# Kernel tuning notes

Measured on AMD Instinct MI355X. Metric: run time of the kernel, lower is better.

Reference implementation:

```python
import jax, jax.numpy as jnp
import numpy as np

# pywt db3 analysis filters (dec_lo, dec_hi)
DB3_LO = np.array([0.035226291882100656, -0.08544127388224149, -0.13501102001039084,
                   0.4598775021193313, 0.8068915093133388, 0.3326705529509569], dtype=np.float32)
DB3_HI = np.array([-0.3326705529509569, 0.8068915093133388, -0.4598775021193313,
                   -0.13501102001039084, 0.08544127388224149, 0.035226291882100656], dtype=np.float32)
L_FILT = 6
J_LEVELS = 3
EPS = 1e-8


def _dwt_level(x):
    """One analysis level, zero-padding ('zero' mode, matches pywt/pytorch_wavelets).
    x: [B, N] -> (low [B, M], high [B, M]) with M = floor((N + L - 1) / 2).
    Uses true convolution (filters flipped) of the full zero-extended signal,
    downsampled at odd full-conv indices, implemented as one strided conv."""
    k = jnp.asarray(np.stack([DB3_LO[::-1], DB3_HI[::-1]])[:, None, :])  # [2,1,L]
    y = jax.lax.conv_general_dilated(x[:, None, :].astype(jnp.float32), k,
                                     window_strides=(2,),
                                     padding=[(L_FILT - 2, L_FILT - 1)])  # [B,2,M]
    return y[:, 0, :], y[:, 1, :]


def _dwt_stats(signals):
    """signals: [B, N]. Returns (mean of final low band, sum over levels of L2 norm
    of each high band) per row -- exactly what the torch loop computes per entity."""
    x = signals
    high_energy = jnp.zeros(signals.shape[0], signals.dtype)
    for _ in range(J_LEVELS):
        lo, hi = _dwt_level(x)
        high_energy = high_energy + jnp.sqrt(jnp.sum(hi * hi, axis=-1))
        x = lo
    return jnp.mean(x, axis=-1), high_energy


def _dirichlet_weight(key, low, high):
    a1 = jnp.clip(low, 1e-6)
    a2 = jnp.clip(high, 1e-6)
    s = a1 + a2
    a1, a2 = a1 / s, a2 / s
    # first component of Dirichlet([10*a1, 10*a2]) ~ Beta(10*a1, 10*a2)
    return jax.random.beta(key, 10.0 * a1, 10.0 * a2)


def setup_inputs() -> dict:
    key = jax.random.key(0)
    k1, k2, k3 = jax.random.split(key, 3)
    U, I, NNZ = 16384, 8192, 1000000
    user_idx = jax.random.randint(k1, (NNZ,), 0, U, dtype=jnp.int32)
    item_idx = jax.random.randint(k2, (NNZ,), 0, I, dtype=jnp.int32)
    values = jax.random.uniform(k3, (NNZ,), dtype=jnp.float32)
    return {"user_idx": user_idx, "item_idx": item_idx, "values": values,
            "num_users": U, "num_items": I}


def reference(user_idx, item_idx, values, num_users, num_items):
    # item popularity
    counts = jax.ops.segment_sum(jnp.ones_like(values), item_idx, num_segments=num_items)
    log_counts = jnp.log1p(counts)
    pop = jax.ops.segment_sum(values * log_counts[item_idx], item_idx, num_segments=num_items)
    pop = pop / (jnp.linalg.norm(pop) + EPS)
    # user activity
    act = jax.ops.segment_sum(values / jnp.log1p(pop[item_idx] + EPS),
                              user_idx, num_segments=num_users)
    act = act / (jnp.linalg.norm(act) + EPS)
    # batched dense signals + DWT (replaces per-entity python loop)
    Su = jnp.zeros((num_users, num_items), values.dtype).at[user_idx, item_idx].set(
        values * (1.0 + act[user_idx]))
    u_low, u_high = _dwt_stats(Su)
    Si = jnp.zeros((num_items, num_users), values.dtype).at[item_idx, user_idx].set(
        values * (1.0 + pop[item_idx]))
    i_low, i_high = _dwt_stats(Si)
    ku, ki = jax.random.split(jax.random.key(42))
    upw = _dirichlet_weight(ku, u_low, u_high)
    ipw = _dirichlet_weight(ki, i_low, i_high)
    return (upw, 1.0 - upw, ipw, 1.0 - ipw, act, pop)
```

## Files before the change

### kernel.cpp

```cpp
#include <hip/hip_runtime.h>
#include <stdint.h>

#define PARTITIONABLE 1

typedef unsigned long long ull;

#define NUM_U 16384
#define NUM_I 8192
#define CAP_U 160
#define CAP_I 256

#define OFF_UPW 0
#define OFF_UMW 16384
#define OFF_IPW 32768
#define OFF_IMW 40960
#define OFF_ACT 49152
#define OFF_POP 65536

struct K2 { uint32_t a, b; };

__host__ __device__ inline void tf2x32(uint32_t k0, uint32_t k1, uint32_t& x0, uint32_t& x1) {
  const uint32_t ks2 = k0 ^ k1 ^ 0x1BD11BDAu;
  x0 += k0; x1 += k1;
#define TF_R(r) { x0 += x1; x1 = (x1 << (r)) | (x1 >> (32 - (r))); x1 ^= x0; }
  TF_R(13) TF_R(15) TF_R(26) TF_R(6)
  x0 += k1; x1 += ks2 + 1u;
  TF_R(17) TF_R(29) TF_R(16) TF_R(24)
  x0 += ks2; x1 += k0 + 2u;
  TF_R(13) TF_R(15) TF_R(26) TF_R(6)
  x0 += k0; x1 += k1 + 3u;
  TF_R(17) TF_R(29) TF_R(16) TF_R(24)
  x0 += k1; x1 += ks2 + 4u;
  TF_R(13) TF_R(15) TF_R(26) TF_R(6)
  x0 += ks2; x1 += k0 + 5u;
#undef TF_R
}

__host__ __device__ inline K2 tf_enc(K2 k, uint32_t x0, uint32_t x1) {
  tf2x32(k.a, k.b, x0, x1);
  K2 r; r.a = x0; r.b = x1; return r;
}

__host__ __device__ inline void split2(K2 k, K2& c0, K2& c1) {
#if PARTITIONABLE
  c0 = tf_enc(k, 0u, 0u);
  c1 = tf_enc(k, 0u, 1u);
#else
  K2 p = tf_enc(k, 0u, 2u);
  K2 q = tf_enc(k, 1u, 3u);
  c0.a = p.a; c0.b = q.a;
  c1.a = p.b; c1.b = q.b;
#endif
}

__device__ inline void split3(K2 k, K2& c0, K2& c1, K2& c2) {
#if PARTITIONABLE
  c0 = tf_enc(k, 0u, 0u);
  c1 = tf_enc(k, 0u, 1u);
  c2 = tf_enc(k, 0u, 2u);
#else
  K2 p = tf_enc(k, 0u, 3u);
  K2 q = tf_enc(k, 1u, 4u);
  K2 r = tf_enc(k, 2u, 5u);
  c0.a = p.a; c0.b = q.a;
  c1.a = r.a; c1.b = p.b;
  c2.a = q.b; c2.b = r.b;
#endif
}

__device__ inline uint32_t draw_bits(K2 k) {
  K2 e = tf_enc(k, 0u, 0u);
#if PARTITIONABLE
  return e.a ^ e.b;
#else
  return e.a;
#endif
}

__device__ inline K2 elem_key(K2 k, uint32_t i, uint32_t B) {
#if PARTITIONABLE
  return tf_enc(k, 0u, i);
#else
  if (i < (B >> 1)) {
    K2 p = tf_enc(k, 2u * i, B + 2u * i);
    K2 q = tf_enc(k, 2u * i + 1u, B + 2u * i + 1u);
    K2 r; r.a = p.a; r.b = q.a; return r;
  } else {
    uint32_t j = 2u * i - B;
    K2 p = tf_enc(k, j, 2u * i);
    K2 q = tf_enc(k, j + 1u, 2u * i + 1u);
    K2 r; r.a = p.b; r.b = q.b; return r;
  }
#endif
}

__device__ inline float u01_bits(uint32_t b) {
  return __uint_as_float((b >> 9) | 0x3F800000u) - 1.0f;
}

__device__ inline float erfinv_f32(float x) {
  float w = -log1pf(-x * x);
  float p;
  if (w < 5.0f) {
    w = w - 2.5f;
    p = 2.81022636e-08f;
    p = fmaf(p, w, 3.43273939e-07f);
    p = fmaf(p, w, -3.5233877e-06f);
    p = fmaf(p, w, -4.39150654e-06f);
    p = fmaf(p, w, 0.00021858087f);
    p = fmaf(p, w, -0.00125372503f);
    p = fmaf(p, w, -0.00417768164f);
    p = fmaf(p, w, 0.246640727f);
    p = fmaf(p, w, 1.50140941f);
  } else {
    w = sqrtf(w) - 3.0f;
    p = -0.000200214257f;
    p = fmaf(p, w, 0.000100950558f);
    p = fmaf(p, w, 0.00134934322f);
    p = fmaf(p, w, -0.00367342844f);
    p = fmaf(p, w, 0.00573950773f);
    p = fmaf(p, w, -0.0076224613f);
    p = fmaf(p, w, 0.00943887047f);
    p = fmaf(p, w, 1.00167406f);
    p = fmaf(p, w, 2.83297682f);
  }
  return p * x;
}

__device__ float log_gamma_sample(K2 key, float alpha_orig) {
  const bool boost = (alpha_orig >= 1.0f);
  const float alpha = boost ? alpha_orig : (alpha_orig + 1.0f);
  const float d = alpha - 0.33333334f;
  const float c = 0.33333334f / sqrtf(d);

  K2 k0, sub;
  split2(key, k0, sub);
  const float u_boost = u01_bits(draw_bits(sub));

  K2 kcur = k0;
  float X = 0.0f, V = 1.0f, U = 2.0f;
  while ((U >= 1.0f - 0.0331f * (X * X)) &&
         (logf(U) >= X * 0.5f + d * ((1.0f - V) + logf(V)))) {
    K2 knext, xk, Uk;
    split3(kcur, knext, xk, Uk);
    kcur = knext;
    float x, v;
    K2 ik = xk;
    do {
      K2 in0, isub;
      split2(ik, in0, isub);
      ik = in0;
      float f = u01_bits(draw_bits(isub));
      float u = fmaxf(-0.99999994f, f * 2.0f + (-0.99999994f));
      x = 1.41421356f * erfinv_f32(u);
      v = 1.0f + x * c;
    } while (v <= 0.0f);
    X = x * x;
    V = (v * v) * v;
    U = u01_bits(draw_bits(Uk));
  }
  float lg = logf(d * V);
  if (!boost) lg += log1pf(-u_boost) / alpha_orig;
  return lg;
}


__global__ __launch_bounds__(256) void init_kernel(ull* __restrict__ nrm2pair,
                                                   ull* __restrict__ fills, int nfill) {
  int i = blockIdx.x * 256 + threadIdx.x;
  if (i < 2) nrm2pair[i] = 0ull;
  if (i < nfill) fills[i] = 0ull;
}

__global__ __launch_bounds__(256) void count_fill_kernel(
    const int* __restrict__ user, const int* __restrict__ item, int n,
    int* __restrict__ fu, int* __restrict__ fi,
    uint32_t* __restrict__ lu, uint32_t* __restrict__ li) {
  for (int k = blockIdx.x * 256 + threadIdx.x; k < n; k += gridDim.x * 256) {
    int it = item[k];
    int q = atomicAdd(&fi[it], 1);
    if (q < CAP_I) li[(size_t)it * CAP_I + q] = (uint32_t)k;
    int u = user[k];
    int p = atomicAdd(&fu[u], 1);
    if (p < CAP_U) lu[(size_t)u * CAP_U + p] = (uint32_t)k;
  }
}

__global__ __launch_bounds__(256) void pop_wave_kernel(
    const int* __restrict__ fi, const uint32_t* __restrict__ li,
    const float* __restrict__ values,
    float* __restrict__ pop, double* __restrict__ nrm2) {
  __shared__ float red[4];
  int lane = threadIdx.x & 63, wid = threadIdx.x >> 6;
  int i = blockIdx.x * 4 + wid;
  int cnt = fi[i];
  int cr = cnt < CAP_I ? cnt : CAP_I;
  long long s = 0;
  for (int e = lane; e < cr; e += 64)
    s += (long long)llrintf(values[li[(size_t)i * CAP_I + e]] * 4294967296.0f);
  for (int o = 32; o > 0; o >>= 1) s += __shfl_down(s, o);
  if (lane == 0) {
    float svf = (float)((double)(ull)s * (1.0 / 4294967296.0));
    float p = svf * log1pf((float)cnt);
    pop[i] = p;
    red[wid] = p * p;
  }
  __syncthreads();
  if (threadIdx.x == 0)
    atomicAdd(nrm2, (double)(red[0] + red[1] + red[2] + red[3]));
}

__global__ __launch_bounds__(256) void act_wave_kernel(
    const int* __restrict__ fu, const uint32_t* __restrict__ lu,
    const int* __restrict__ item, const float* __restrict__ values,
    const float* __restrict__ pop, const double* __restrict__ nrm2_pop,
    float* __restrict__ act, double* __restrict__ nrm2) {
  __shared__ float red[4];
  int lane = threadIdx.x & 63, wid = threadIdx.x >> 6;
  int u = blockIdx.x * 4 + wid;
  int cnt = fu[u];
  int cr = cnt < CAP_U ? cnt : CAP_U;
  const float nrmp = sqrtf((float)(*nrm2_pop));
  const float dnp = nrmp + 1e-8f;
  long long s = 0;
  for (int e = lane; e < cr; e += 64) {
    uint32_t k = lu[(size_t)u * CAP_U + e];
    float pn = pop[item[k]] / dnp;
    float term = values[k] / log1pf(pn + 1e-8f);
    s += (long long)llrintf(term * 16777216.0f);
  }
  for (int o = 32; o > 0; o >>= 1) s += __shfl_down(s, o);
  if (lane == 0) {
    float a = (float)((double)(ull)s * (1.0 / 16777216.0));
    act[u] = a;
    red[wid] = a * a;
  }
  __syncthreads();
  if (threadIdx.x == 0)
    atomicAdd(nrm2, (double)(red[0] + red[1] + red[2] + red[3]));
}

__device__ inline uint32_t evencomp(uint32_t x) {
  x = (x | (x >> 1)) & 0x55555555u;
  x = (x | (x >> 1)) & 0x33333333u;
  x = (x | (x >> 2)) & 0x0F0F0F0Fu;
  x = (x | (x >> 4)) & 0x00FF00FFu;
  x = (x | (x >> 8)) & 0x0000FFFFu;
  return x;
}
template <int NWIN>
__device__ inline uint32_t hword(const uint32_t* B, int i) {
  uint32_t a = (2 * i < NWIN) ? B[2 * i] : 0u;
  uint32_t b = (2 * i + 1 < NWIN) ? B[2 * i + 1] : 0u;
  return evencomp(a) | (evencomp(b) << 16);
}
template <int NWIN>
__device__ inline uint32_t tword(const uint32_t* B, int w) {
  uint32_t h = hword<NWIN>(B, w);
  uint32_t hp = (w > 0) ? hword<NWIN>(B, w - 1) : 0u;
  return h | (h << 1) | (h << 2) | (hp >> 31) | (hp >> 30);
}

template <int NWORDS>
__device__ inline int scan_bits(const uint32_t* __restrict__ W, uint16_t* __restrict__ P,
                                int tid, int* __restrict__ isc, int* __restrict__ tot) {
  constexpr int WPT = (NWORDS + 255) / 256;
  __syncthreads();
  uint32_t w[WPT];
  int v = 0;
#pragma unroll
  for (int j = 0; j < WPT; ++j) {
    int idx = tid * WPT + j;
    w[j] = (idx < NWORDS) ? W[idx] : 0u;
    v += __popc(w[j]);
  }
  int lane = tid & 63, wid = tid >> 6;
  int incl = v;
  for (int off = 1; off < 64; off <<= 1) {
    int y = __shfl_up(incl, off, 64);
    if (lane >= off) incl += y;
  }
  if (lane == 63) isc[wid] = incl;
  __syncthreads();
  int base = 0;
  for (int ww = 0; ww < wid; ++ww) base += isc[ww];
  int run = base + incl - v;
#pragma unroll
  for (int j = 0; j < WPT; ++j) {
    int idx = tid * WPT + j;
    if (idx < NWORDS) P[idx] = (uint16_t)run;
    run += __popc(w[j]);
  }
  if (tid == 255) *tot = run;
  __syncthreads();
  return *tot;
}

template <int NWORDS>
__device__ inline void build_wl(const uint32_t* __restrict__ T, const uint16_t* __restrict__ P,
                                uint16_t* __restrict__ wl, int tid) {
  for (int w = tid; w < NWORDS; w += 256) {
    uint32_t bits = T[w];
    int r0 = P[w], i = 0;
    while (bits) {
      int b = __ffs(bits) - 1; bits &= bits - 1u;
      wl[r0 + i] = (uint16_t)((w << 5) + b);
      ++i;
    }
  }
}

template <int NIN>
__device__ inline void gather6(const uint32_t* __restrict__ B, const uint16_t* __restrict__ P,
                               const float* __restrict__ V, int m,
                               float& lo_o, float& hi_o) {
  int c0 = 2 * m - 4; c0 = c0 < 0 ? 0 : c0;
  int c1 = 2 * m + 1; c1 = c1 > NIN - 1 ? NIN - 1 : c1;
  int w0 = c0 >> 5, w1 = c1 >> 5;
  uint32_t b0 = B[w0];
  uint32_t mlo = ~((1u << (c0 & 31)) - 1u);
  uint32_t mhi = (uint32_t)(((uint64_t)1u << ((c1 & 31) + 1)) - 1u);
  uint32_t sel0, sel1; uint32_t b1 = 0;
  if (w1 == w0) { sel0 = b0 & mlo & mhi; sel1 = 0u; }
  else { b1 = B[w1]; sel0 = b0 & mlo; sel1 = b1 & mhi; }
  float tv0 = 0.0f, tv1 = 0.0f, tv2 = 0.0f, tv3 = 0.0f, tv4 = 0.0f, tv5 = 0.0f;
  int tp1 = 2 * m + 1;
  uint32_t s = sel0;
  while (s) {
    int b = __ffs(s) - 1; s &= s - 1u;
    int c = (w0 << 5) + b;
    int idx = (int)P[w0] + __popc(b0 & ((1u << b) - 1u));
    float v = V[idx];
    int t = tp1 - c;
    if (t == 0) tv0 = v; else if (t == 1) tv1 = v; else if (t == 2) tv2 = v;
    else if (t == 3) tv3 = v; else if (t == 4) tv4 = v; else tv5 = v;
  }
  s = sel1;
  while (s) {
    int b = __ffs(s) - 1; s &= s - 1u;
    int c = (w1 << 5) + b;
    int idx = (int)P[w1] + __popc(b1 & ((1u << b) - 1u));
    float v = V[idx];
    int t = tp1 - c;
    if (t == 0) tv0 = v; else if (t == 1) tv1 = v; else if (t == 2) tv2 = v;
    else if (t == 3) tv3 = v; else if (t == 4) tv4 = v; else tv5 = v;
  }
  float lo = 0.0f, hi = 0.0f;
  lo += 0.035226291882100656f * tv0;  hi += -0.3326705529509569f * tv0;
  lo += -0.08544127388224149f * tv1;  hi += 0.8068915093133388f * tv1;
  lo += -0.13501102001039084f * tv2;  hi += -0.4598775021193313f * tv2;
  lo += 0.4598775021193313f * tv3;    hi += -0.13501102001039084f * tv3;
  lo += 0.8068915093133388f * tv4;    hi += 0.08544127388224149f * tv4;
  lo += 0.3326705529509569f * tv5;    hi += 0.035226291882100656f * tv5;
  lo_o = lo; hi_o = hi;
}

__device__ inline int rank_of(const uint32_t* __restrict__ B, const uint16_t* __restrict__ P,
                              int m) {
  int w = m >> 5;
  return (int)P[w] + __popc(B[w] & ((1u << (m & 31)) - 1u));
}

constexpr int align4c(int x) { return (x + 3) & ~3; }
constexpr int cmax(int a, int b) { return a > b ? a : b; }

constexpr int dwt_shm_bytes(int NCOLS, int M1, int M2, int M3, int CAP) {
  int NW = NCOLS / 32, NW1 = (M1 + 31) / 32, NW2 = (M2 + 31) / 32, NW3 = (M3 + 31) / 32;
  int SZ_RB = cmax(cmax(align4c(NW * 4 + NW * 2), align4c(NW2 * 4 + 4 * CAP * 2)),
                   align4c(5 * CAP * 2));
  int SZ_RC = cmax(align4c(NW1 * 4 + NW1 * 2), align4c(NW3 * 4 + NW3 * 2 + NW2 * 2));
  return (M1 + 12) * 4 + CAP * 4 + SZ_RB + SZ_RC + align4c(3 * CAP * 2) + 64;
}

template <int NCOLS, int M1, int M2, int M3, int CAP>
__global__ __launch_bounds__(256) void dwt_rows_kernel(
    const uint32_t* __restrict__ klist, const int* __restrict__ rowlen,
    const int* __restrict__ colsrc, const float* __restrict__ values,
    const float* __restrict__ scale_raw, const double* __restrict__ nrm2,
    float* __restrict__ low_out, float* __restrict__ high_out,
    float* __restrict__ out, int outoff) {
  static_assert(CAP <= 256, "register-carry staging requires CAP <= blockDim");
  constexpr int NW = NCOLS / 32;
  constexpr int NW1 = (M1 + 31) / 32;
  constexpr int NW2 = (M2 + 31) / 32;
  constexpr int NW3 = (M3 + 31) / 32;
  constexpr uint32_t MK1 = (M1 & 31) ? ((1u << (M1 & 31)) - 1u) : 0xFFFFFFFFu;
  constexpr uint32_t MK2 = (M2 & 31) ? ((1u << (M2 & 31)) - 1u) : 0xFFFFFFFFu;
  constexpr uint32_t MK3 = (M3 & 31) ? ((1u << (M3 & 31)) - 1u) : 0xFFFFFFFFu;
  constexpr int SZ_RB = cmax(cmax(align4c(NW * 4 + NW * 2), align4c(NW2 * 4 + 4 * CAP * 2)),
                             align4c(5 * CAP * 2));
  constexpr int SZ_RC = cmax(align4c(NW1 * 4 + NW1 * 2), align4c(NW3 * 4 + NW3 * 2 + NW2 * 2));

  extern __shared__ char smroot[];
  float* buf = (float*)smroot;
  char* pA = smroot + (M1 + 12) * 4;
  int* slot = (int*)pA;
  float* sval = (float*)pA;
  char* pB = pA + CAP * 4;
  uint32_t* bitmap = (uint32_t*)pB;
  uint16_t* prefix = (uint16_t*)(pB + NW * 4);
  uint32_t* T2 = (uint32_t*)pB;
  uint16_t* wl2 = (uint16_t*)(pB + NW2 * 4);
  uint16_t* wl3 = (uint16_t*)pB;
  char* pC = pB + SZ_RB;
  uint32_t* T1 = (uint32_t*)pC;
  uint16_t* p1 = (uint16_t*)(pC + NW1 * 4);
  uint32_t* T3 = (uint32_t*)pC;
  uint16_t* p3 = (uint16_t*)(pC + NW3 * 4);
  uint16_t* p2 = (uint16_t*)(pC + NW3 * 4 + NW3 * 2);
  char* pD = pC + SZ_RC;
  uint16_t* wl1 = (uint16_t*)pD;
  char* pE = pD + align4c(3 * CAP * 2);
  int* isc = (int*)pE;
  int* tot = isc + 4;
  float* red = (float*)pE;

  const int r = blockIdx.x;
  const int tid = threadIdx.x;
  const float nrm = sqrtf((float)(*nrm2));
  const float snv = scale_raw[r] / (nrm + 1e-8f);
  const float scale = 1.0f + snv;
  if (tid == 0) out[outoff + r] = snv;
  int n = rowlen[r];
  if (n > CAP) n = CAP;

  {
    constexpr int NB4 = (M1 + 12) / 4;
    float4 z; z.x = 0.0f; z.y = 0.0f; z.z = 0.0f; z.w = 0.0f;
    for (int i = tid; i < NB4; i += 256) ((float4*)buf)[i] = z;
    for (int i = NB4 * 4 + tid; i < M1 + 12; i += 256) buf[i] = 0.0f;
  }
  for (int i = tid; i < NW; i += 256) bitmap[i] = 0u;
  if (tid < CAP) slot[tid] = 0;
  __syncthreads();

  const bool have = tid < n;
  uint32_t my_k = 0; int my_c = 0; float my_v = 0.0f;
  if (have) {
    my_k = klist[(size_t)r * CAP + tid];
    my_c = colsrc[my_k];
    my_v = values[my_k] * scale;
    atomicOr(&bitmap[my_c >> 5], 1u << (my_c & 31));
  }
  scan_bits<NW>(bitmap, prefix, tid, isc, tot);

  int my_rank = 0;
  if (have) {
    my_rank = rank_of(bitmap, prefix, my_c);
    atomicMax(&slot[my_rank], (int)my_k + 1);
  }
  __syncthreads();

  if (have && slot[my_rank] == (int)my_k + 1) sval[my_rank] = my_v;
  for (int w = tid; w < NW1; w += 256) {
    uint32_t t = tword<NW>(bitmap, w);
    if (w == NW1 - 1) t &= MK1;
    T1[w] = t;
  }
  const int n1 = scan_bits<NW1>(T1, p1, tid, isc, tot);
  build_wl<NW1>(T1, p1, wl1, tid);
  __syncthreads();

  float h1 = 0.0f;
  for (int idx = tid; idx < n1; idx += 256) {
    int m = wl1[idx];
    float lo, hi;
    gather6<NCOLS>(bitmap, prefix, sval, m, lo, hi);
    buf[4 + m] = lo;
    h1 += hi * hi;
  }
  __syncthreads();

  for (int w = tid; w < NW2; w += 256) {
    uint32_t t = tword<NW1>(T1, w);
    if (w == NW2 - 1) t &= MK2;
    T2[w] = t;
  }
  const int n2 = scan_bits<NW2>(T2, p2, tid, isc, tot);
  build_wl<NW2>(T2, p2, wl2, tid);
  for (int w = tid; w < NW3; w += 256) {
    uint32_t t = tword<NW2>(T2, w);
    if (w == NW3 - 1) t &= MK3;
    T3[w] = t;
  }
  __syncthreads();

  float h2 = 0.0f;
  {
    int nb = (n2 + 255) >> 8;
    for (int b = 0; b < nb; ++b) {
      int idx = (b << 8) + tid;
      bool ok = idx < n2;
      int m = ok ? wl2[idx] : 0;
      const float* s = buf + 2 * m + 5;
      float x0 = s[0], x1 = s[-1], x2 = s[-2], x3 = s[-3], x4 = s[-4], x5 = s[-5];
      __syncthreads();
      if (ok) {
        float lo = 0.0f, hi = 0.0f;
        lo += 0.035226291882100656f * x0;  hi += -0.3326705529509569f * x0;
        lo += -0.08544127388224149f * x1;  hi += 0.8068915093133388f * x1;
        lo += -0.13501102001039084f * x2;  hi += -0.4598775021193313f * x2;
        lo += 0.4598775021193313f * x3;    hi += -0.13501102001039084f * x3;
        lo += 0.8068915093133388f * x4;    hi += 0.08544127388224149f * x4;
        lo += 0.3326705529509569f * x5;    hi += 0.035226291882100656f * x5;
        buf[4 + m] = lo;
        h2 += hi * hi;
      }
    }
  }
  __syncthreads();
  for (int idx = tid; idx < n1; idx += 256) {
    int m = wl1[idx];
    if (m < M2 && !((T2[m >> 5] >> (m & 31)) & 1u)) buf[4 + m] = 0.0f;
  }
  if (tid < 8) buf[4 + M2 + tid] = 0.0f;

  const int n3 = scan_bits<NW3>(T3, p3, tid, isc, tot);
  build_wl<NW3>(T3, p3, wl3, tid);
  __syncthreads();

  float h3 = 0.0f, slo = 0.0f;
  for (int idx = tid; idx < n3; idx += 256) {
    int m = wl3[idx];
    const float* s = buf + 2 * m + 5;
    float x0 = s[0], x1 = s[-1], x2 = s[-2], x3 = s[-3], x4 = s[-4], x5 = s[-5];
    float lo = 0.0f, hi = 0.0f;
    lo += 0.035226291882100656f * x0;  hi += -0.3326705529509569f * x0;
    lo += -0.08544127388224149f * x1;  hi += 0.8068915093133388f * x1;
    lo += -0.13501102001039084f * x2;  hi += -0.4598775021193313f * x2;
    lo += 0.4598775021193313f * x3;    hi += -0.13501102001039084f * x3;
    lo += 0.8068915093133388f * x4;    hi += 0.08544127388224149f * x4;
    lo += 0.3326705529509569f * x5;    hi += 0.035226291882100656f * x5;
    slo += lo;
    h3 += hi * hi;
  }

  for (int o = 32; o > 0; o >>= 1) {
    h1 += __shfl_down(h1, o);
    h2 += __shfl_down(h2, o);
    h3 += __shfl_down(h3, o);
    slo += __shfl_down(slo, o);
  }
  __syncthreads();
  int w = tid >> 6, lane = tid & 63;
  if (lane == 0) { red[w] = h1; red[4 + w] = h2; red[8 + w] = h3; red[12 + w] = slo; }
  __syncthreads();
  if (tid == 0) {
    float s1 = red[0] + red[1] + red[2] + red[3];
    float s2 = red[4] + red[5] + red[6] + red[7];
    float s3 = red[8] + red[9] + red[10] + red[11];
    float sl = red[12] + red[13] + red[14] + red[15];
    low_out[r] = sl / (float)M3;
    high_out[r] = sqrtf(s1) + sqrtf(s2) + sqrtf(s3);
  }
}

__global__ __launch_bounds__(64) void gamma_kernel(
    const float* __restrict__ u_low, const float* __restrict__ u_high,
    const float* __restrict__ i_low, const float* __restrict__ i_high,
    float* __restrict__ lgbuf, K2 kAu, K2 kBu, K2 kAi, K2 kBi) {
  const int TOT = NUM_U + NUM_I;
  int t = blockIdx.x * 64 + threadIdx.x;
  if (t >= 2 * TOT) return;
  int ab = t >= TOT ? 1 : 0;
  int ent = ab ? t - TOT : t;
  float low, high;
  K2 key;
  if (ent < NUM_U) {
    low = u_low[ent]; high = u_high[ent];
    key = elem_key(ab ? kBu : kAu, (uint32_t)ent, (uint32_t)NUM_U);
  } else {
    int j = ent - NUM_U;
    low = i_low[j]; high = i_high[j];
    key = elem_key(ab ? kBi : kAi, (uint32_t)j, (uint32_t)NUM_I);
  }
  float a1 = fmaxf(low, 1e-6f);
  float a2 = fmaxf(high, 1e-6f);
  float s = a1 + a2;
  float alpha = ab ? (10.0f * (a2 / s)) : (10.0f * (a1 / s));
  lgbuf[t] = log_gamma_sample(key, alpha);
}

__global__ __launch_bounds__(256) void combine_kernel(
    const float* __restrict__ lgbuf, float* __restrict__ out) {
  const int TOT = NUM_U + NUM_I;
  int t = blockIdx.x * 256 + threadIdx.x;
  if (t >= TOT) return;
  float lga = lgbuf[t];
  float lgb = lgbuf[TOT + t];
  float m = fmaxf(lga, lgb);
  float na = expf(lga - m);
  float nb = expf(lgb - m);
  float w = na / (na + nb);
  int o0, o1;
  if (t < NUM_U) { o0 = OFF_UPW + t; o1 = OFF_UMW + t; }
  else { int j = t - NUM_U; o0 = OFF_IPW + j; o1 = OFF_IMW + j; }
  out[o0] = w;
  out[o1] = 1.0f - w;
}

extern "C" void kernel_launch(void* const* d_in, const int* in_sizes, int n_in,
                              void* d_out, int out_size, void* d_ws, size_t ws_size,
                              hipStream_t stream) {
  const int* user_idx = (const int*)d_in[0];
  const int* item_idx = (const int*)d_in[1];
  const float* values = (const float*)d_in[2];
  const int NNZ = in_sizes[0];

  char* ws = (char*)d_ws;
  double* nrm2_pop = (double*)(ws + 0);
  double* nrm2_act = (double*)(ws + 8);
  float* lgbuf = (float*)(ws + 16);
  float* pop = (float*)(ws + 229392);
  float* act = (float*)(ws + 262160);
  int* fill_u = (int*)(ws + 327696);
  int* fill_i = (int*)(ws + 393232);
  float* u_low = (float*)(ws + 426000);
  float* u_high = (float*)(ws + 491536);
  float* i_low = (float*)(ws + 557072);
  float* i_high = (float*)(ws + 589840);
  uint32_t* klist_u = (uint32_t*)(ws + 622608);
  uint32_t* klist_i = (uint32_t*)(ws + 11108368);
  float* out = (float*)d_out;

  K2 root; root.a = 0u; root.b = 42u;
  K2 ku, ki, kAu, kBu, kAi, kBi;
  split2(root, ku, ki);
  split2(ku, kAu, kBu);
  split2(ki, kAi, kBi);

  init_kernel<<<48, 256, 0, stream>>>((ull*)ws, (ull*)(ws + 327696), 98304 / 8);
  count_fill_kernel<<<1024, 256, 0, stream>>>(user_idx, item_idx, NNZ,
                                              fill_u, fill_i, klist_u, klist_i);
  pop_wave_kernel<<<NUM_I / 4, 256, 0, stream>>>(fill_i, klist_i, values, pop, nrm2_pop);
  act_wave_kernel<<<NUM_U / 4, 256, 0, stream>>>(fill_u, klist_u, item_idx, values,
                                                 pop, nrm2_pop, act, nrm2_act);

  constexpr int U_SHM = dwt_shm_bytes(8192, 4098, 2051, 1028, CAP_U);
  constexpr int I_SHM = dwt_shm_bytes(16384, 8194, 4099, 2052, CAP_I);
  hipFuncSetAttribute((const void*)dwt_rows_kernel<8192, 4098, 2051, 1028, CAP_U>,
                      hipFuncAttributeMaxDynamicSharedMemorySize, U_SHM);
  hipFuncSetAttribute((const void*)dwt_rows_kernel<16384, 8194, 4099, 2052, CAP_I>,
                      hipFuncAttributeMaxDynamicSharedMemorySize, I_SHM);

  dwt_rows_kernel<8192, 4098, 2051, 1028, CAP_U><<<NUM_U, 256, U_SHM, stream>>>(
      klist_u, fill_u, item_idx, values, act, nrm2_act, u_low, u_high, out, OFF_ACT);
  dwt_rows_kernel<16384, 8194, 4099, 2052, CAP_I><<<NUM_I, 256, I_SHM, stream>>>(
      klist_i, fill_i, user_idx, values, pop, nrm2_pop, i_low, i_high, out, OFF_POP);

  const int TOT2 = 2 * (NUM_U + NUM_I);
  gamma_kernel<<<(TOT2 + 63) / 64, 64, 0, stream>>>(
      u_low, u_high, i_low, i_high, lgbuf, kAu, kBu, kAi, kBi);
  combine_kernel<<<(NUM_U + NUM_I + 255) / 256, 256, 0, stream>>>(lgbuf, out);
}
```

Before: 403.9 us.

## Build per-row index lists in LDS buckets instead of global atomics

Replaces the global-atomic count/fill kernel with a bucketed kernel. Each block owns 128 item rows or 128 user rows and scans the entire index array with int4 loads. It builds counts and index lists with LDS atomics, then writes them back to global memory with coalesced stores. This removes random global atomics and scattered list writes, and drops the zeroing of the fill counters. In exchange, every one of the 192 blocks rereads the full 1M-entry index array, and each block needs about 128KB of LDS.

```diff
diff --git a/kernel.cpp b/kernel.cpp
--- a/kernel.cpp
+++ b/kernel.cpp
@@ -9,6 +9,11 @@
 #define NUM_I 8192
 #define CAP_U 160
 #define CAP_I 256
+
+#define IB_ROWS 128
+#define UB_ROWS 128
+#define N_IBUCKET (NUM_I / IB_ROWS)
+#define N_UBUCKET (NUM_U / UB_ROWS)
 
 #define OFF_UPW 0
 #define OFF_UMW 16384
@@ -165,25 +170,61 @@
 }
 
 
-__global__ __launch_bounds__(256) void init_kernel(ull* __restrict__ nrm2pair,
-                                                   ull* __restrict__ fills, int nfill) {
-  int i = blockIdx.x * 256 + threadIdx.x;
+__global__ __launch_bounds__(256) void init_kernel(ull* __restrict__ nrm2pair) {
+  int i = threadIdx.x;
   if (i < 2) nrm2pair[i] = 0ull;
-  if (i < nfill) fills[i] = 0ull;
-}
-
-__global__ __launch_bounds__(256) void count_fill_kernel(
+}
+
+__global__ __launch_bounds__(256) void bucket_fill_kernel(
     const int* __restrict__ user, const int* __restrict__ item, int n,
     int* __restrict__ fu, int* __restrict__ fi,
     uint32_t* __restrict__ lu, uint32_t* __restrict__ li) {
-  for (int k = blockIdx.x * 256 + threadIdx.x; k < n; k += gridDim.x * 256) {
-    int it = item[k];
-    int q = atomicAdd(&fi[it], 1);
-    if (q < CAP_I) li[(size_t)it * CAP_I + q] = (uint32_t)k;
-    int u = user[k];
-    int p = atomicAdd(&fu[u], 1);
-    if (p < CAP_U) lu[(size_t)u * CAP_U + p] = (uint32_t)k;
-  }
+  extern __shared__ uint32_t lsm[];
+  const int bid = blockIdx.x;
+  const int tid = threadIdx.x;
+  const bool is_item = bid < N_IBUCKET;
+  const int rows = is_item ? IB_ROWS : UB_ROWS;
+  const int cap = is_item ? CAP_I : CAP_U;
+  const int base = is_item ? bid * IB_ROWS : (bid - N_IBUCKET) * UB_ROWS;
+  const int* __restrict__ src = is_item ? item : user;
+  uint32_t* cnt = lsm;
+  uint32_t* list = lsm + rows;
+
+  for (int i = tid; i < rows; i += 256) cnt[i] = 0u;
+  __syncthreads();
+
+  const int4* src4 = (const int4*)src;
+  const int n4 = n >> 2;
+  int k4 = tid;
+  if (k4 < n4) {
+    int4 v = src4[k4];
+    for (;;) {
+      int kn = k4 + 256;
+      int4 vn;
+      if (kn < n4) vn = src4[kn];
+      int k0 = k4 << 2;
+      int r0 = v.x - base, r1 = v.y - base, r2 = v.z - base, r3 = v.w - base;
+      if ((unsigned)r0 < (unsigned)rows) { uint32_t q = atomicAdd(&cnt[r0], 1u); if ((int)q < cap) list[r0 * cap + (int)q] = (uint32_t)k0; }
+      if ((unsigned)r1 < (unsigned)rows) { uint32_t q = atomicAdd(&cnt[r1], 1u); if ((int)q < cap) list[r1 * cap + (int)q] = (uint32_t)(k0 + 1); }
+      if ((unsigned)r2 < (unsigned)rows) { uint32_t q = atomicAdd(&cnt[r2], 1u); if ((int)q < cap) list[r2 * cap + (int)q] = (uint32_t)(k0 + 2); }
+      if ((unsigned)r3 < (unsigned)rows) { uint32_t q = atomicAdd(&cnt[r3], 1u); if ((int)q < cap) list[r3 * cap + (int)q] = (uint32_t)(k0 + 3); }
+      if (kn >= n4) break;
+      k4 = kn; v = vn;
+    }
+  }
+  for (int k = (n4 << 2) + tid; k < n; k += 256) {
+    int r = src[k] - base;
+    if ((unsigned)r < (unsigned)rows) { uint32_t q = atomicAdd(&cnt[r], 1u); if ((int)q < cap) list[r * cap + (int)q] = (uint32_t)k; }
+  }
+  __syncthreads();
+
+  uint32_t* gl = (is_item ? li : lu) + (size_t)base * cap;
+  const int w4 = (rows * cap) >> 2;
+  int4* gl4 = (int4*)gl;
+  const int4* ls4 = (const int4*)list;
+  for (int i = tid; i < w4; i += 256) gl4[i] = ls4[i];
+  int* fc = (is_item ? fi : fu) + base;
+  for (int i = tid; i < rows; i += 256) fc[i] = (int)cnt[i];
 }
 
 __global__ __launch_bounds__(256) void pop_wave_kernel(
@@ -629,9 +670,14 @@
   split2(ku, kAu, kBu);
   split2(ki, kAi, kBi);
 
-  init_kernel<<<48, 256, 0, stream>>>((ull*)ws, (ull*)(ws + 327696), 98304 / 8);
-  count_fill_kernel<<<1024, 256, 0, stream>>>(user_idx, item_idx, NNZ,
-                                              fill_u, fill_i, klist_u, klist_i);
+  init_kernel<<<1, 256, 0, stream>>>((ull*)ws);
+
+  constexpr int BF_SHM = IB_ROWS * 4 + IB_ROWS * CAP_I * 4;
+  hipFuncSetAttribute((const void*)bucket_fill_kernel,
+                      hipFuncAttributeMaxDynamicSharedMemorySize, BF_SHM);
+  bucket_fill_kernel<<<N_IBUCKET + N_UBUCKET, 256, BF_SHM, stream>>>(
+      user_idx, item_idx, NNZ, fill_u, fill_i, klist_u, klist_i);
+
   pop_wave_kernel<<<NUM_I / 4, 256, 0, stream>>>(fill_i, klist_i, values, pop, nrm2_pop);
   act_wave_kernel<<<NUM_U / 4, 256, 0, stream>>>(fill_u, klist_u, item_idx, values,
                                                  pop, nrm2_pop, act, nrm2_act);
```

Measured after the change: 605.0 us. 49.8% more time.
